# Performance work log

Measured on AMD Instinct MI355X. Metric: run time of the kernel, lower is better.

The kernel has to match this reference:

```python
import jax, jax.numpy as jnp
import numpy as np

B, N, E, M = 512, 101, 128, 8
DK = E // M  # 16
EPS = 1e-5

def _bn(x, g, b):
    # torch BatchNorm1d in train mode on (B, E, N): per-channel stats over batch+city dims, biased var
    mu = jnp.mean(x, axis=(0, 1))
    var = jnp.mean((x - mu) ** 2, axis=(0, 1))
    return (x - mu) * jax.lax.rsqrt(var + EPS) * g + b

def setup_inputs() -> dict:
    key = jax.random.key(0)
    ks = jax.random.split(key, 24)
    sc = 1.0 / np.sqrt(E)
    inp = {
        's': jax.random.uniform(ks[0], (B, N, 2), jnp.float32),
        'd': jax.random.randint(ks[1], (B, N, 1), 0, 10),
        'e_w': jax.random.normal(ks[2], (3, E), jnp.float32) * sc,
        'e_b': jax.random.normal(ks[3], (E,), jnp.float32) * sc,
        'ep_w': jax.random.normal(ks[4], (2, E), jnp.float32) * sc,
        'ep_b': jax.random.normal(ks[5], (E,), jnp.float32) * sc,
        'Wq': jax.random.normal(ks[6], (3, E, E), jnp.float32) * sc,
        'bq': jax.random.normal(ks[7], (3, E), jnp.float32) * sc,
        'Wk': jax.random.normal(ks[8], (3, E, E), jnp.float32) * sc,
        'bk': jax.random.normal(ks[9], (3, E), jnp.float32) * sc,
        'Wv': jax.random.normal(ks[10], (3, E, E), jnp.float32) * sc,
        'bv': jax.random.normal(ks[11], (3, E), jnp.float32) * sc,
        'Wo': jax.random.normal(ks[12], (3, E, E), jnp.float32) * sc,
        'bo': jax.random.normal(ks[13], (3, E), jnp.float32) * sc,
        'Wf1': jax.random.normal(ks[14], (3, E, 4 * E), jnp.float32) * sc,
        'bf1': jax.random.normal(ks[15], (3, 4 * E), jnp.float32) * sc,
        'Wf2': jax.random.normal(ks[16], (3, 4 * E, E), jnp.float32) * sc,
        'bf2': jax.random.normal(ks[17], (3, E), jnp.float32) * sc,
        'g1': jnp.ones((3, E), jnp.float32),
        'be1': jnp.zeros((3, E), jnp.float32),
        'g2': jnp.ones((3, E), jnp.float32),
        'be2': jnp.zeros((3, E), jnp.float32),
    }
    return inp

def reference(s, d, e_w, e_b, ep_w, ep_b, Wq, bq, Wk, bk, Wv, bv, Wo, bo,
              Wf1, bf1, Wf2, bf2, g1, be1, g2, be2):
    # node embedding: cat(coords, demand) -> Linear(3,E); depot row uses Linear(2,E)
    sss = jnp.concatenate([s, d.astype(s.dtype)], axis=2)          # (B,N,3)
    node = sss @ e_w + e_b                                         # (B,N,E)
    node = node.at[:, 0, :].set(s[:, 0, :] @ ep_w + ep_b)
    x = node
    inv_sqrt_dk = 1.0 / (DK ** 0.5)
    for i in range(3):
        res = x
        q = (x @ Wq[i] + bq[i]).reshape(B, N, M, DK)
        k = (x @ Wk[i] + bk[i]).reshape(B, N, M, DK)
        v = (x @ Wv[i] + bv[i]).reshape(B, N, M, DK)
        # scores[b,i,j,h] = <q_i, k_j> per head (source does expand*mul*sum)
        scores = jnp.einsum('bihd,bjhd->bijh', q, k) * inv_sqrt_dk  # (B,N,N,M)
        a = jax.nn.softmax(scores, axis=2)                          # over keys j
        o = jnp.einsum('bijh,bjhd->bihd', a, v).reshape(B, N, E)
        x = _bn(o @ Wo[i] + bo[i] + res, g1[i], be1[i])
        ff = jax.nn.relu(x @ Wf1[i] + bf1[i]) @ Wf2[i] + bf2[i]
        x = _bn(x + ff, g2[i], be2[i])
    return x
```

## Files before the change

kernel.cpp:

```cpp
#include <hip/hip_runtime.h>
#include <hip/hip_fp16.h>
#include <stdint.h>

#define TROWS 51712
#define NCITY 101
#define BATCH 512
#define EDIM  128
#define NBH   4096

using half_t = _Float16;
typedef __attribute__((ext_vector_type(8))) _Float16 h8;
typedef __attribute__((ext_vector_type(4))) _Float16 h4;
typedef __attribute__((ext_vector_type(4))) float   f32x4;

typedef __attribute__((address_space(1))) const unsigned int gu32;
typedef __attribute__((address_space(3))) unsigned int lu32;
static __device__ __forceinline__ void async16(const void* g, const void* l) {
    __builtin_amdgcn_global_load_lds((gu32*)g, (lu32*)(uint32_t)(uintptr_t)l, 16, 0, 0);
}

static __device__ __forceinline__ int swz_col(int c, int row) {
    return (c & ~31) | ((((c >> 3) ^ (row >> 1)) & 3) << 3) | (c & 7);
}

__global__ __launch_bounds__(256)
void prep_kernel(const float* __restrict__ Wq, const float* __restrict__ Wk,
                 const float* __restrict__ Wv, const float* __restrict__ Wo,
                 const float* __restrict__ Wf1, const float* __restrict__ Wf2,
                 const float* __restrict__ bq, const float* __restrict__ bk,
                 const float* __restrict__ bv,
                 half_t* __restrict__ wqkv, half_t* __restrict__ wo,
                 half_t* __restrict__ wf1, half_t* __restrict__ wf2,
                 float* __restrict__ bqkv)
{
    const int which = blockIdx.y;
    const int gid = blockIdx.x * 256 + threadIdx.x;
    if (which <= 2) {
        if (gid >= 3 * 128 * 128) return;
        const float* src = (which == 0) ? Wq : (which == 1) ? Wk : Wv;
        int l = gid >> 14, r = gid & 16383, k = r >> 7, n = r & 127;
        wqkv[(size_t)l * 49152 + which * 16384 + n * 128 + swz_col(k, n)] = (half_t)src[gid];
    } else if (which == 3) {
        if (gid >= 3 * 128 * 128) return;
        int l = gid >> 14, r = gid & 16383, k = r >> 7, n = r & 127;
        wo[(size_t)l * 16384 + n * 128 + swz_col(k, n)] = (half_t)Wo[gid];
    } else if (which == 4) {
        if (gid >= 3 * 65536) return;
        int l = gid >> 16, u = gid & 65535;
        int j = u >> 13, kc = (u >> 11) & 3, n = (u >> 5) & 63, hp = u & 31;
        int k = kc * 32 + ((((hp >> 3) ^ (n >> 1)) & 3) << 3) + (hp & 7);
        wf1[(size_t)l * 65536 + u] = (half_t)Wf1[(size_t)(l * 128 + k) * 512 + j * 64 + n];
    } else if (which == 5) {
        if (gid >= 3 * 65536) return;
        int l = gid >> 16, u = gid & 65535;
        int j = u >> 13, kc = (u >> 12) & 1, n = (u >> 5) & 127, hp = u & 31;
        int kh = j * 64 + kc * 32 + ((((hp >> 3) ^ (n >> 1)) & 3) << 3) + (hp & 7);
        wf2[(size_t)l * 65536 + u] = (half_t)Wf2[(size_t)(l * 512 + kh) * 128 + n];
    } else {
        if (gid >= 3 * 384) return;
        int l = gid / 384, c = gid - l * 384;
        float v = (c < 128) ? bq[l * 128 + c]
                : (c < 256) ? bk[l * 128 + c - 128]
                            : bv[l * 128 + c - 256];
        bqkv[gid] = v;
    }
}

__global__ __launch_bounds__(256)
void embed_kernel(const float* __restrict__ s, const int* __restrict__ d,
                  const float* __restrict__ e_w, const float* __restrict__ e_b,
                  const float* __restrict__ ep_w, const float* __restrict__ ep_b,
                  half_t* __restrict__ xh)
{
    int gid = blockIdx.x * 256 + threadIdx.x;
    int row = gid >> 7;
    int c   = gid & 127;
    int b = row / NCITY;
    int n = row - b * NCITY;
    const float* sp = s + ((size_t)b * NCITY + n) * 2;
    float v;
    if (n == 0) {
        v = sp[0] * ep_w[c] + sp[1] * ep_w[128 + c] + ep_b[c];
    } else {
        float dv = (float)d[b * NCITY + n];
        v = sp[0] * e_w[c] + sp[1] * e_w[128 + c] + dv * e_w[256 + c] + e_b[c];
    }
    xh[(size_t)row * 128 + swz_col(c, row)] = (half_t)v;
}

__global__ __launch_bounds__(512, 1)
void layer_attn(const half_t* __restrict__ xh, const half_t* __restrict__ wqkv,
                const float* __restrict__ bqkv, const half_t* __restrict__ wo,
                const float* __restrict__ bo, half_t* __restrict__ y16,
                float* __restrict__ stats)
{
    __shared__ alignas(16) half_t sO[112 * 136];
    __shared__ alignas(16) half_t sQKV[3][8][112 * 16];
    half_t* sX = sO;

    const int b   = blockIdx.x;
    const int tid = threadIdx.x;
    const int wave = tid >> 6, lane = tid & 63;
    const int quad = lane >> 4, l16 = lane & 15;

    if (tid < 448) {
        int row = tid >> 2, kc = tid & 3;
        h8* dst = (h8*)&sX[kc * 3584 + row * 32];
        if (row < NCITY) {
            size_t grow = (size_t)b * NCITY + row;
            const h8* src = (const h8*)(xh + grow * 128 + kc * 32);
            int xf = (int)(((grow >> 1) ^ (row >> 1)) & 3);
            h8 v0 = src[0], v1 = src[1], v2 = src[2], v3 = src[3];
            dst[0 ^ xf] = v0;
            dst[1 ^ xf] = v1;
            dst[2 ^ xf] = v2;
            dst[3 ^ xf] = v3;
        } else {
            h8 z = {};
            dst[0] = z; dst[1] = z; dst[2] = z; dst[3] = z;
        }
    }
    __syncthreads();

    const int hn  = wave * 16 + l16;
    const int nsw = (hn >> 1) & 3;
    h8 bfr[3][4];
    float bv3[3];
    #pragma unroll
    for (int which = 0; which < 3; ++which) {
        const half_t* wrow = wqkv + which * 16384 + (size_t)hn * 128;
        #pragma unroll
        for (int kc = 0; kc < 4; ++kc)
            bfr[which][kc] = *(const h8*)(wrow + kc * 32 + (((quad ^ nsw) & 3) << 3));
        bv3[which] = bqkv[which * 128 + hn];
    }
    #pragma unroll
    for (int mi = 0; mi < 7; ++mi) {
        h8 af[4];
        #pragma unroll
        for (int kc = 0; kc < 4; ++kc) {
            int r = mi * 16 + l16;
            af[kc] = *(const h8*)(&sX[kc * 3584 + r * 32 + (((quad ^ (r >> 1)) & 3) << 3)]);
        }
        #pragma unroll
        for (int which = 0; which < 3; ++which) {
            f32x4 a = {};
            #pragma unroll
            for (int kc = 0; kc < 4; ++kc)
                a = __builtin_amdgcn_mfma_f32_16x16x32_f16(af[kc], bfr[which][kc], a, 0, 0, 0);
            half_t* dstL = &sQKV[which][wave][0];
            #pragma unroll
            for (int r = 0; r < 4; ++r) {
                int tok = mi * 16 + quad * 4 + r;
                int dsw = l16 ^ (((tok >> 2) & 1) << 3);
                dstL[tok * 16 + dsw] = (half_t)(a[r] + bv3[which]);
            }
        }
    }
    __syncthreads();

    const half_t* qb = &sQKV[0][wave][0];
    const half_t* kb = &sQKV[1][wave][0];
    const half_t* vb = &sQKV[2][wave][0];
    const int kflip = (l16 >> 2) & 1;

    const int s0 = (((quad & 1) * 2)    ) * 16 + l16;
    const int s1 = (((quad & 1) * 2) + 1) * 16 + l16;
    const bool hi2 = (quad >> 1) != 0;

    h8 kf[7];
    #pragma unroll
    for (int jt = 0; jt < 7; ++jt) {
        kf[jt] = (h8){};
        if (quad < 2)
            kf[jt] = *(const h8*)(kb + (jt * 16 + l16) * 16 + ((quad ^ kflip) << 3));
    }
    h8 vt[4];
    #pragma unroll
    for (int p = 0; p < 4; ++p)
        #pragma unroll
        for (int jj = 0; jj < 8; ++jj) {
            int tok = p * 32 + quad * 8 + jj;
            vt[p][jj] = vb[tok * 16 + (l16 ^ (((jj >> 2) & 1) << 3))];
        }

    const int ocol = hn;

    for (int it = 0; it < 7; ++it) {
        h8 qf = {};
        if (quad < 2)
            qf = *(const h8*)(qb + (it * 16 + l16) * 16 + ((quad ^ kflip) << 3));

        f32x4 S[7];
        #pragma unroll
        for (int jt = 0; jt < 7; ++jt) {
            f32x4 a = {};
            a = __builtin_amdgcn_mfma_f32_16x16x32_f16(kf[jt], qf, a, 0, 0, 0);
            S[jt] = a;
        }
        float m = -1e30f;
        #pragma unroll
        for (int jt = 0; jt < 7; ++jt)
            #pragma unroll
            for (int r = 0; r < 4; ++r) {
                int jg = jt * 16 + quad * 4 + r;
                float sv = (jg < NCITY) ? S[jt][r] * 0.25f : -1e30f;
                S[jt][r] = sv;
                m = fmaxf(m, sv);
            }
        m = fmaxf(m, __shfl_xor(m, 16));
        m = fmaxf(m, __shfl_xor(m, 32));
        float sum = 0.0f;
        #pragma unroll
        for (int jt = 0; jt < 7; ++jt)
            #pragma unroll
            for (int r = 0; r < 4; ++r) {
                float e = __expf(S[jt][r] - m);
                S[jt][r] = e;
                sum += e;
            }
        sum += __shfl_xor(sum, 16);
        sum += __shfl_xor(sum, 32);
        float inv = 1.0f / sum;
        #pragma unroll
        for (int jt = 0; jt < 7; ++jt)
            #pragma unroll
            for (int r = 0; r < 4; ++r) S[jt][r] *= inv;

        f32x4 O = {};
        #pragma unroll
        for (int p = 0; p < 4; ++p) {
            float pj[8];
            #pragma unroll
            for (int r = 0; r < 4; ++r) {
                float a0 = __shfl(S[2 * p][r],     s0);
                float b0 = __shfl(S[2 * p + 1][r], s0);
                float a1 = __shfl(S[2 * p][r],     s1);
                float b1 = __shfl(S[2 * p + 1][r], s1);
                pj[r]     = hi2 ? b0 : a0;
                pj[4 + r] = hi2 ? b1 : a1;
            }
            h8 ph;
            #pragma unroll
            for (int jj = 0; jj < 8; ++jj)
                ph[jj] = (half_t)pj[jj];
            O = __builtin_amdgcn_mfma_f32_16x16x32_f16(ph, vt[p], O, 0, 0, 0);
        }
        #pragma unroll
        for (int r = 0; r < 4; ++r) {
            int q = it * 16 + quad * 4 + r;
            int g = (ocol >> 3) ^ ((q & 8) >> 2);
            sO[q * 136 + g * 8 + (ocol & 7)] = (half_t)O[r];
        }
    }
    __syncthreads();

    h8 bfr2[4];
    {
        const half_t* wrow = wo + (size_t)ocol * 128;
        const int nsw2 = (ocol >> 1) & 3;
        #pragma unroll
        for (int kc = 0; kc < 4; ++kc)
            bfr2[kc] = *(const h8*)(wrow + kc * 32 + (((quad ^ nsw2) & 3) << 3));
    }
    f32x4 acc[7];
    #pragma unroll
    for (int mi = 0; mi < 7; ++mi) {
        acc[mi] = (f32x4){};
        int row = mi * 16 + l16;
        int swr = (row & 8) >> 2;
        #pragma unroll
        for (int kc = 0; kc < 4; ++kc) {
            h8 af = *(const h8*)(&sO[row * 136 + (((kc * 4 + quad) ^ swr) << 3)]);
            acc[mi] = __builtin_amdgcn_mfma_f32_16x16x32_f16(af, bfr2[kc], acc[mi], 0, 0, 0);
        }
    }
    float bvv = bo[ocol];
    float s = 0.0f, ss = 0.0f;
    #pragma unroll
    for (int mi = 0; mi < 7; ++mi) {
        #pragma unroll
        for (int r = 0; r < 4; ++r) {
            int q = mi * 16 + quad * 4 + r;
            if (q < NCITY) {
                size_t grow = (size_t)b * NCITY + q;
                float o = acc[mi][r] + bvv + (float)xh[grow * 128 + swz_col(ocol, (int)grow)];
                y16[grow * 128 + ocol] = (half_t)o;
                s += o; ss += o * o;
            }
        }
    }
    s  += __shfl_xor(s, 16);  s  += __shfl_xor(s, 32);
    ss += __shfl_xor(ss, 16); ss += __shfl_xor(ss, 32);
    if (quad == 0) {
        atomicAdd(&stats[ocol], s);
        atomicAdd(&stats[128 + ocol], ss);
    }
}

__global__ __launch_bounds__(512, 4)
void ff_fused(half_t* __restrict__ y16, const float* __restrict__ st1,
              const float* __restrict__ g1, const float* __restrict__ be1,
              const half_t* __restrict__ w1, const half_t* __restrict__ w2,
              const float* __restrict__ bf1, const float* __restrict__ bf2,
              float* __restrict__ stats)
{
    __shared__ alignas(16) half_t sX[4][128 * 32];
    __shared__ alignas(16) half_t sW1f[8192];
    __shared__ alignas(16) half_t sW2f[8192];
    __shared__ alignas(16) half_t sH[2][128 * 32];

    const int tid  = threadIdx.x;
    const int wave = tid >> 6, lane = tid & 63;
    const int quad = lane >> 4, l16 = lane & 15;
    const int m0 = blockIdx.x * 128;
    const int wr = wave >> 1;
    const int wc = wave & 1;

    const float invN = 1.0f / (float)TROWS;
    const int so = wave * 512 + lane * 8;

    h8 rw1a = *(const h8*)(w1 + so);
    h8 rw1b = *(const h8*)(w1 + so + 4096);
    h8 rw2a = *(const h8*)(w2 + so);
    h8 rw2b = *(const h8*)(w2 + so + 4096);

    float* sBN = (float*)&sW1f[0];
    if (tid < 128) {
        float mean = st1[tid] * invN;
        float var  = st1[128 + tid] * invN - mean * mean;
        float scl  = g1[tid] * rsqrtf(var + 1e-5f);
        sBN[tid]       = scl;
        sBN[128 + tid] = be1[tid] - mean * scl;
    }
    __syncthreads();

    {
        const int row = tid >> 2;
        const int q   = tid & 3;
        const int qs  = ((q ^ (row >> 1)) & 3) << 3;
        const half_t* src = y16 + (size_t)(m0 + row) * 128 + q * 8;
        #pragma unroll
        for (int kc = 0; kc < 4; ++kc) {
            h8 v = *(const h8*)(src + kc * 32);
            h8 xv;
            #pragma unroll
            for (int r = 0; r < 8; ++r) {
                int c = kc * 32 + q * 8 + r;
                xv[r] = (half_t)((float)v[r] * sBN[c] + sBN[128 + c]);
            }
            *(h8*)(&sX[kc][row * 32 + qs]) = xv;
        }
    }

    f32x4 acc2[2][4] = {};

    for (int j = 0; j < 8; ++j) {
        asm volatile("s_waitcnt lgkmcnt(0)" ::: "memory");
        __builtin_amdgcn_s_barrier();
        __builtin_amdgcn_sched_barrier(0);
        *(h8*)(&sW1f[so])        = rw1a;
        *(h8*)(&sW1f[so + 4096]) = rw1b;
        *(h8*)(&sW2f[so])        = rw2a;
        *(h8*)(&sW2f[so + 4096]) = rw2b;
        asm volatile("s_waitcnt lgkmcnt(0)" ::: "memory");
        __builtin_amdgcn_s_barrier();
        __builtin_amdgcn_sched_barrier(0);
        if (j < 7) {
            const half_t* w1n = w1 + (size_t)(j + 1) * 8192;
            const half_t* w2n = w2 + (size_t)(j + 1) * 8192;
            rw1a = *(const h8*)(w1n + so);
            rw1b = *(const h8*)(w1n + so + 4096);
            rw2a = *(const h8*)(w2n + so);
            rw2b = *(const h8*)(w2n + so + 4096);
        }

        f32x4 acc1[2][2] = {};
        #pragma unroll
        for (int kc = 0; kc < 4; ++kc) {
            h8 af[2], bf[2];
            #pragma unroll
            for (int mi = 0; mi < 2; ++mi) {
                int r = wr * 32 + mi * 16 + l16;
                af[mi] = *(const h8*)(&sX[kc][r * 32 + (((quad ^ (r >> 1)) & 3) << 3)]);
            }
            #pragma unroll
            for (int ni = 0; ni < 2; ++ni) {
                int n = wc * 32 + ni * 16 + l16;
                bf[ni] = *(const h8*)(&sW1f[kc * 2048 + n * 32 + (((quad ^ (n >> 1)) & 3) << 3)]);
            }
            #pragma unroll
            for (int mi = 0; mi < 2; ++mi)
            #pragma unroll
            for (int ni = 0; ni < 2; ++ni)
                acc1[mi][ni] = __builtin_amdgcn_mfma_f32_16x16x32_f16(af[mi], bf[ni], acc1[mi][ni], 0, 0, 0);
        }
        #pragma unroll
        for (int ni = 0; ni < 2; ++ni) {
            int c = wc * 32 + ni * 16 + l16;
            float bvv = bf1[j * 64 + c];
            int kc2 = c >> 5, c5 = c & 31;
            #pragma unroll
            for (int mi = 0; mi < 2; ++mi)
            #pragma unroll
            for (int r = 0; r < 4; ++r) {
                int row = wr * 32 + mi * 16 + quad * 4 + r;
                float v = acc1[mi][ni][r] + bvv;
                v = v > 0.0f ? v : 0.0f;
                int hsw = (c5 & 7) | ((((c5 >> 3) ^ (row >> 1)) & 3) << 3);
                sH[kc2][row * 32 + hsw] = (half_t)v;
            }
        }
        asm volatile("s_waitcnt lgkmcnt(0)" ::: "memory");
        __builtin_amdgcn_s_barrier();
        __builtin_amdgcn_sched_barrier(0);

        #pragma unroll
        for (int kc = 0; kc < 2; ++kc) {
            h8 af[2], bf[4];
            #pragma unroll
            for (int mi = 0; mi < 2; ++mi) {
                int r = wr * 32 + mi * 16 + l16;
                af[mi] = *(const h8*)(&sH[kc][r * 32 + (((quad ^ (r >> 1)) & 3) << 3)]);
            }
            #pragma unroll
            for (int ni = 0; ni < 4; ++ni) {
                int n = wc * 64 + ni * 16 + l16;
                bf[ni] = *(const h8*)(&sW2f[kc * 4096 + n * 32 + (((quad ^ (n >> 1)) & 3) << 3)]);
            }
            #pragma unroll
            for (int mi = 0; mi < 2; ++mi)
            #pragma unroll
            for (int ni = 0; ni < 4; ++ni)
                acc2[mi][ni] = __builtin_amdgcn_mfma_f32_16x16x32_f16(af[mi], bf[ni], acc2[mi][ni], 0, 0, 0);
        }
    }

    __syncthreads();
    float* red = (float*)&sH[0][0];

    #pragma unroll
    for (int ni = 0; ni < 4; ++ni) {
        int col = wc * 64 + ni * 16 + l16;
        float bvv = bf2[col];
        int kc = col >> 5, c5 = col & 31;
        float s = 0.0f, ss = 0.0f;
        #pragma unroll
        for (int mi = 0; mi < 2; ++mi) {
            #pragma unroll
            for (int r = 0; r < 4; ++r) {
                int rowl = wr * 32 + mi * 16 + quad * 4 + r;
                int hsw = (c5 & 7) | ((((c5 >> 3) ^ (rowl >> 1)) & 3) << 3);
                float xv = (float)sX[kc][rowl * 32 + hsw];
                float o = acc2[mi][ni][r] + bvv + xv;
                y16[(size_t)(m0 + rowl) * 128 + col] = (half_t)o;
                s += o; ss += o * o;
            }
        }
        s  += __shfl_xor(s, 16);  s  += __shfl_xor(s, 32);
        ss += __shfl_xor(ss, 16); ss += __shfl_xor(ss, 32);
        if (quad == 0) {
            red[wave * 64 + ni * 16 + l16]       = s;
            red[512 + wave * 64 + ni * 16 + l16] = ss;
        }
    }
    __syncthreads();
    if (tid < 256) {
        int a   = tid >> 7;
        int col = tid & 127;
        int wcc = col >> 6, nii = (col >> 4) & 3, lx = col & 15;
        float t = 0.0f;
        #pragma unroll
        for (int w = 0; w < 4; ++w)
            t += red[a * 512 + (w * 2 + wcc) * 64 + nii * 16 + lx];
        atomicAdd(&stats[a * 128 + col], t);
    }
}

__global__ __launch_bounds__(256)
void bn_apply(const h8* __restrict__ y, const float* __restrict__ stats,
              const float* __restrict__ g, const float* __restrict__ be,
              half_t* __restrict__ xh, float* __restrict__ dst32)
{
    __shared__ float sh[256];
    const int tid = threadIdx.x;
    if (tid < 128) {
        const float invN = 1.0f / (float)TROWS;
        float mean = stats[tid] * invN;
        float var  = stats[128 + tid] * invN - mean * mean;
        float inv  = rsqrtf(var + 1e-5f);
        float scl  = g[tid] * inv;
        sh[tid]       = scl;
        sh[128 + tid] = be[tid] - mean * scl;
    }
    __syncthreads();

    int gid = blockIdx.x * 256 + tid;
    int row = gid >> 4;
    int gr  = gid & 15;
    int c = gr * 8;
    h8 v = y[gid];
    h8 hv;
    float o[8];
    #pragma unroll
    for (int r = 0; r < 8; ++r) {
        o[r] = (float)v[r] * sh[c + r] + sh[128 + c + r];
        hv[r] = (half_t)o[r];
    }
    int grp = (gr & ~3) | ((gr ^ (row >> 1)) & 3);
    *reinterpret_cast<h8*>(xh + (size_t)row * 128 + grp * 8) = hv;
    if (dst32) {
        f32x4 lo = { o[0], o[1], o[2], o[3] };
        f32x4 hi = { o[4], o[5], o[6], o[7] };
        ((f32x4*)dst32)[gid * 2]     = lo;
        ((f32x4*)dst32)[gid * 2 + 1] = hi;
    }
}

extern "C" void kernel_launch(void* const* d_in, const int* in_sizes, int n_in,
                              void* d_out, int out_size, void* d_ws, size_t ws_size,
                              hipStream_t stream)
{
    const float* s    = (const float*)d_in[0];
    const int*   dd   = (const int*)d_in[1];
    const float* e_w  = (const float*)d_in[2];
    const float* e_b  = (const float*)d_in[3];
    const float* ep_w = (const float*)d_in[4];
    const float* ep_b = (const float*)d_in[5];
    const float* Wq   = (const float*)d_in[6];
    const float* bq   = (const float*)d_in[7];
    const float* Wk   = (const float*)d_in[8];
    const float* bk   = (const float*)d_in[9];
    const float* Wv   = (const float*)d_in[10];
    const float* bv   = (const float*)d_in[11];
    const float* Wo   = (const float*)d_in[12];
    const float* bo   = (const float*)d_in[13];
    const float* Wf1  = (const float*)d_in[14];
    const float* bf1  = (const float*)d_in[15];
    const float* Wf2  = (const float*)d_in[16];
    const float* bf2  = (const float*)d_in[17];
    const float* g1   = (const float*)d_in[18];
    const float* be1  = (const float*)d_in[19];
    const float* g2   = (const float*)d_in[20];
    const float* be2  = (const float*)d_in[21];

    char* ws = (char*)d_ws;
    size_t off = 0;
    auto alloc = [&](size_t bytes) -> void* {
        void* p = ws + off;
        off += (bytes + 255) & ~(size_t)255;
        return p;
    };
    half_t* y16   = (half_t*)alloc((size_t)TROWS * 128 * 2);
    half_t* xh    = (half_t*)alloc((size_t)TROWS * 128 * 2);
    half_t* wqkv  = (half_t*)alloc((size_t)3 * 384 * 128 * 2);
    half_t* wo    = (half_t*)alloc((size_t)3 * 128 * 128 * 2);
    half_t* wf1   = (half_t*)alloc((size_t)3 * 512 * 128 * 2);
    half_t* wf2   = (half_t*)alloc((size_t)3 * 128 * 512 * 2);
    float*  bqkv  = (float*) alloc((size_t)3 * 384 * 4);
    float*  stats = (float*) alloc(6 * 256 * 4);

    dim3 blk(256);

    hipMemsetAsync(stats, 0, 6 * 256 * 4, stream);

    prep_kernel<<<dim3(768, 7), blk, 0, stream>>>(Wq, Wk, Wv, Wo, Wf1, Wf2, bq, bk, bv,
                                                  wqkv, wo, wf1, wf2, bqkv);

    embed_kernel<<<dim3(TROWS * 128 / 256), blk, 0, stream>>>(s, dd, e_w, e_b, ep_w, ep_b, xh);

    for (int l = 0; l < 3; ++l) {
        float* st1 = stats + (size_t)(l * 2) * 256;
        float* st2 = stats + (size_t)(l * 2 + 1) * 256;
        layer_attn<<<dim3(BATCH), dim3(512), 0, stream>>>(xh, wqkv + (size_t)l * 49152,
                                                          bqkv + l * 384,
                                                          wo + (size_t)l * 16384,
                                                          bo + l * 128, y16, st1);
        ff_fused<<<dim3(404), dim3(512), 0, stream>>>(y16, st1, g1 + l * 128, be1 + l * 128,
                                                      wf1 + (size_t)l * 65536, wf2 + (size_t)l * 65536,
                                                      bf1 + l * 512, bf2 + l * 128, st2);
        bn_apply<<<dim3(TROWS * 16 / 256), blk, 0, stream>>>((const h8*)y16, st2,
                                                             g2 + l * 128, be2 + l * 128,
                                                             xh, (l == 2) ? (float*)d_out : nullptr);
    }
}
```

Measured before the change: 391.8 us.

## Fuse BN2 apply into next layer's attention input load and residual

Layers after the first now read the pre-BN activations `y16` directly in `layer_attn`. The attention kernel computes per-channel BN scale and shift from the previous layer's stats and applies them while staging inputs into LDS and when adding the residual. This removes the intermediate `bn_apply` launches and their full read/write pass over the activations; only the final layer still runs `bn_apply`, writing fp32 output. In exchange, the global activation layout becomes unswizzled and the attention kernel does extra per-element multiply-adds and reads y16 in place while overwriting it.

New measurement: 379.0 us. -3.3%, faster.

```diff
diff --git a/kernel.cpp b/kernel.cpp
--- a/kernel.cpp
+++ b/kernel.cpp
@@ -85,40 +85,62 @@
         float dv = (float)d[b * NCITY + n];
         v = sp[0] * e_w[c] + sp[1] * e_w[128 + c] + dv * e_w[256 + c] + e_b[c];
     }
-    xh[(size_t)row * 128 + swz_col(c, row)] = (half_t)v;
+    xh[gid] = (half_t)v;
 }
 
 __global__ __launch_bounds__(512, 1)
-void layer_attn(const half_t* __restrict__ xh, const half_t* __restrict__ wqkv,
-                const float* __restrict__ bqkv, const half_t* __restrict__ wo,
-                const float* __restrict__ bo, half_t* __restrict__ y16,
-                float* __restrict__ stats)
+void layer_attn(const half_t* __restrict__ xsrc, const float* __restrict__ stats0,
+                const float* __restrict__ g0, const float* __restrict__ be0,
+                const half_t* __restrict__ wqkv, const float* __restrict__ bqkv,
+                const half_t* __restrict__ wo, const float* __restrict__ bo,
+                half_t* __restrict__ y16, float* __restrict__ stats)
 {
     __shared__ alignas(16) half_t sO[112 * 136];
     __shared__ alignas(16) half_t sQKV[3][8][112 * 16];
     half_t* sX = sO;
+    float* sBN2 = (float*)&sQKV[0][0][0];
 
     const int b   = blockIdx.x;
     const int tid = threadIdx.x;
     const int wave = tid >> 6, lane = tid & 63;
     const int quad = lane >> 4, l16 = lane & 15;
-
+    const float invN = 1.0f / (float)TROWS;
+
+    if (stats0) {
+        if (tid < 128) {
+            float mean = stats0[tid] * invN;
+            float var  = stats0[128 + tid] * invN - mean * mean;
+            float scl  = g0[tid] * rsqrtf(var + 1e-5f);
+            sBN2[tid]       = scl;
+            sBN2[128 + tid] = be0[tid] - mean * scl;
+        }
+        __syncthreads();
+    }
     if (tid < 448) {
-        int row = tid >> 2, kc = tid & 3;
-        h8* dst = (h8*)&sX[kc * 3584 + row * 32];
+        int row = tid >> 2, q = tid & 3;
+        int qs = ((q ^ (row >> 1)) & 3) << 3;
+        h8 out[4];
         if (row < NCITY) {
-            size_t grow = (size_t)b * NCITY + row;
-            const h8* src = (const h8*)(xh + grow * 128 + kc * 32);
-            int xf = (int)(((grow >> 1) ^ (row >> 1)) & 3);
-            h8 v0 = src[0], v1 = src[1], v2 = src[2], v3 = src[3];
-            dst[0 ^ xf] = v0;
-            dst[1 ^ xf] = v1;
-            dst[2 ^ xf] = v2;
-            dst[3 ^ xf] = v3;
+            const half_t* src = xsrc + ((size_t)b * NCITY + row) * 128 + q * 8;
+            #pragma unroll
+            for (int kc = 0; kc < 4; ++kc) {
+                h8 v = *(const h8*)(src + kc * 32);
+                if (stats0) {
+                    #pragma unroll
+                    for (int r = 0; r < 8; ++r) {
+                        int c = kc * 32 + q * 8 + r;
+                        v[r] = (half_t)((float)v[r] * sBN2[c] + sBN2[128 + c]);
+                    }
+                }
+                out[kc] = v;
+            }
         } else {
             h8 z = {};
-            dst[0] = z; dst[1] = z; dst[2] = z; dst[3] = z;
-        }
+            out[0] = z; out[1] = z; out[2] = z; out[3] = z;
+        }
+        #pragma unroll
+        for (int kc = 0; kc < 4; ++kc)
+            *(h8*)(&sX[kc * 3584 + row * 32 + qs]) = out[kc];
     }
     __syncthreads();
 
@@ -275,6 +297,13 @@
             acc[mi] = __builtin_amdgcn_mfma_f32_16x16x32_f16(af, bfr2[kc], acc[mi], 0, 0, 0);
         }
     }
+    float sclo = 1.0f, shfo = 0.0f;
+    if (stats0) {
+        float mean = stats0[ocol] * invN;
+        float var  = stats0[128 + ocol] * invN - mean * mean;
+        sclo = g0[ocol] * rsqrtf(var + 1e-5f);
+        shfo = be0[ocol] - mean * sclo;
+    }
     float bvv = bo[ocol];
     float s = 0.0f, ss = 0.0f;
     #pragma unroll
@@ -284,7 +313,8 @@
             int q = mi * 16 + quad * 4 + r;
             if (q < NCITY) {
                 size_t grow = (size_t)b * NCITY + q;
-                float o = acc[mi][r] + bvv + (float)xh[grow * 128 + swz_col(ocol, (int)grow)];
+                float xv = (float)xsrc[grow * 128 + ocol] * sclo + shfo;
+                float o = acc[mi][r] + bvv + xv;
                 y16[grow * 128 + ocol] = (half_t)o;
                 s += o; ss += o * o;
             }
@@ -480,7 +510,7 @@
 __global__ __launch_bounds__(256)
 void bn_apply(const h8* __restrict__ y, const float* __restrict__ stats,
               const float* __restrict__ g, const float* __restrict__ be,
-              half_t* __restrict__ xh, float* __restrict__ dst32)
+              float* __restrict__ dst32)
 {
     __shared__ float sh[256];
     const int tid = threadIdx.x;
@@ -496,25 +526,16 @@
     __syncthreads();
 
     int gid = blockIdx.x * 256 + tid;
-    int row = gid >> 4;
-    int gr  = gid & 15;
-    int c = gr * 8;
+    int c = (gid & 15) * 8;
     h8 v = y[gid];
-    h8 hv;
     float o[8];
     #pragma unroll
-    for (int r = 0; r < 8; ++r) {
+    for (int r = 0; r < 8; ++r)
         o[r] = (float)v[r] * sh[c + r] + sh[128 + c + r];
-        hv[r] = (half_t)o[r];
-    }
-    int grp = (gr & ~3) | ((gr ^ (row >> 1)) & 3);
-    *reinterpret_cast<h8*>(xh + (size_t)row * 128 + grp * 8) = hv;
-    if (dst32) {
-        f32x4 lo = { o[0], o[1], o[2], o[3] };
-        f32x4 hi = { o[4], o[5], o[6], o[7] };
-        ((f32x4*)dst32)[gid * 2]     = lo;
-        ((f32x4*)dst32)[gid * 2 + 1] = hi;
-    }
+    f32x4 lo = { o[0], o[1], o[2], o[3] };
+    f32x4 hi = { o[4], o[5], o[6], o[7] };
+    ((f32x4*)dst32)[gid * 2]     = lo;
+    ((f32x4*)dst32)[gid * 2 + 1] = hi;
 }
 
 extern "C" void kernel_launch(void* const* d_in, const int* in_sizes, int n_in,
@@ -572,15 +593,20 @@
     for (int l = 0; l < 3; ++l) {
         float* st1 = stats + (size_t)(l * 2) * 256;
         float* st2 = stats + (size_t)(l * 2 + 1) * 256;
-        layer_attn<<<dim3(BATCH), dim3(512), 0, stream>>>(xh, wqkv + (size_t)l * 49152,
+        const float* st0 = (l == 0) ? nullptr : stats + (size_t)((l - 1) * 2 + 1) * 256;
+        const half_t* xsrc = (l == 0) ? xh : y16;
+        layer_attn<<<dim3(BATCH), dim3(512), 0, stream>>>(xsrc, st0,
+                                                          g2 + (l ? (l - 1) * 128 : 0),
+                                                          be2 + (l ? (l - 1) * 128 : 0),
+                                                          wqkv + (size_t)l * 49152,
                                                           bqkv + l * 384,
                                                           wo + (size_t)l * 16384,
                                                           bo + l * 128, y16, st1);
         ff_fused<<<dim3(404), dim3(512), 0, stream>>>(y16, st1, g1 + l * 128, be1 + l * 128,
                                                       wf1 + (size_t)l * 65536, wf2 + (size_t)l * 65536,
                                                       bf1 + l * 512, bf2 + l * 128, st2);
-        bn_apply<<<dim3(TROWS * 16 / 256), blk, 0, stream>>>((const h8*)y16, st2,
-                                                             g2 + l * 128, be2 + l * 128,
-                                                             xh, (l == 2) ? (float*)d_out : nullptr);
-    }
-}
+    }
+    bn_apply<<<dim3(TROWS * 16 / 256), blk, 0, stream>>>((const h8*)y16, stats + 5 * 256,
+                                                         g2 + 2 * 128, be2 + 2 * 128,
+                                                         (float*)d_out);
+}
```
